# Kernel tuning notes

Measured on AMD Instinct MI355X. Metric: run time of the kernel, lower is better.

## Reference

```python
import jax, jax.numpy as jnp
import numpy as np

WINDOW = 8  # outlier_fraction = 0.125 -> 1 fp column kept per 8-wide window

# XnorBinaryLinear's STEBinary: sign in fwd, identity (straight-through) in bwd
@jax.custom_vjp
def ste_sign(x):
    return jnp.sign(x)

def _ste_fwd(x):
    return jnp.sign(x), None

def _ste_bwd(_, g):
    return (g,)

ste_sign.defvjp(_ste_fwd, _ste_bwd)


def quant_weight(w):
    # XnorBinaryLinear.quant_weight: per-row mean-center, sign, rescale by
    # detached per-row mean absolute value
    mu = jnp.mean(w, axis=-1, keepdims=True)
    wc = w - mu
    scale = jax.lax.stop_gradient(jnp.mean(jnp.abs(wc), axis=-1, keepdims=True))
    return ste_sign(wc) * scale


def binarize_except_outliers(w):
    # Binarize weight, then restore the max-|w| element of each flat 8-wide
    # window to full precision (calibration = argmax of |w| per window,
    # identical to outlier_calibration with L1 metric on first forward).
    wq = quant_weight(w)
    wv = w.reshape(-1, WINDOW)             # [n_windows, 8]
    idx = jnp.argmax(jnp.abs(wv), axis=1)  # [n_windows] outlier column per window
    mask = jnp.arange(WINDOW)[None, :] == idx[:, None]  # one-hot bool mask
    out = jnp.where(mask, wv, wq.reshape(-1, WINDOW))
    return out.reshape(w.shape)


def setup_inputs() -> dict:
    key = jax.random.key(0)
    k1, k2, k3 = jax.random.split(key, 3)
    x = jax.random.normal(k1, (4, 2048, 4096), dtype=jnp.float32)
    weight = jax.random.normal(k2, (4096, 4096), dtype=jnp.float32) * 0.02
    bias = jax.random.normal(k3, (4096,), dtype=jnp.float32) * 0.02
    return {"x": x, "weight": weight, "bias": bias}


def reference(x, weight, bias):
    w = binarize_except_outliers(weight)     # [OC, IC]
    return jnp.einsum('bsi,oi->bso', x, w) + bias
```

## Files before the change

kernel.cpp:

```cpp
#include <hip/hip_runtime.h>
#include <stdint.h>

#define M_DIM 8192
#define N_DIM 4096
#define K_DIM 4096

#define BM 128
#define BN 128
#define BK 32

typedef float v4f __attribute__((ext_vector_type(4)));
typedef __bf16 v8bf __attribute__((ext_vector_type(8)));

typedef __attribute__((address_space(3))) uint32_t lds_u32_t;
typedef const __attribute__((address_space(1))) uint32_t glb_u32_t;

__device__ inline uint16_t f2bf(float f) {
    union { float f; uint32_t u; } v; v.f = f;
    uint32_t r = v.u + 0x7fffu + ((v.u >> 16) & 1u);
    return (uint16_t)(r >> 16);
}

__global__ __launch_bounds__(256) void cvt_x(const float* __restrict__ x,
                                             uint16_t* __restrict__ xb,
                                             long long n8) {
    long long i = (long long)blockIdx.x * 256 + threadIdx.x;
    if (i >= n8) return;
    const float4* x4 = (const float4*)x;
    float4 a = x4[2 * i];
    float4 b = x4[2 * i + 1];
    union { uint16_t h[8]; uint4 u; } o;
    o.h[0] = f2bf(a.x); o.h[1] = f2bf(a.y); o.h[2] = f2bf(a.z); o.h[3] = f2bf(a.w);
    o.h[4] = f2bf(b.x); o.h[5] = f2bf(b.y); o.h[6] = f2bf(b.z); o.h[7] = f2bf(b.w);
    ((uint4*)xb)[i] = o.u;
}

__global__ __launch_bounds__(256) void make_weff(const float* __restrict__ w,
                                                 uint16_t* __restrict__ weff) {
    __shared__ double red[4];
    int row  = blockIdx.x;
    int tid  = threadIdx.x;
    int lane = tid & 63;
    int wid  = tid >> 6;

    const float* wr = w + (size_t)row * K_DIM;
    const float4* w4 = (const float4*)wr + tid * 4;
    float4 r0 = w4[0], r1 = w4[1], r2 = w4[2], r3 = w4[3];
    float v[16] = { r0.x, r0.y, r0.z, r0.w, r1.x, r1.y, r1.z, r1.w,
                    r2.x, r2.y, r2.z, r2.w, r3.x, r3.y, r3.z, r3.w };

    double s = 0.0;
#pragma unroll
    for (int j = 0; j < 16; j++) s += (double)v[j];
#pragma unroll
    for (int off = 32; off > 0; off >>= 1) s += __shfl_down(s, off);
    if (lane == 0) red[wid] = s;
    __syncthreads();
    double mu = (red[0] + red[1] + red[2] + red[3]) * (1.0 / 4096.0);
    __syncthreads();

    double sa = 0.0;
#pragma unroll
    for (int j = 0; j < 16; j++) sa += fabs((double)v[j] - mu);
#pragma unroll
    for (int off = 32; off > 0; off >>= 1) sa += __shfl_down(sa, off);
    if (lane == 0) red[wid] = sa;
    __syncthreads();
    double scale = (red[0] + red[1] + red[2] + red[3]) * (1.0 / 4096.0);

    float scf = (float)scale;
    union { uint16_t h[16]; uint4 u[2]; } o;
#pragma unroll
    for (int w2 = 0; w2 < 2; w2++) {
        int base = w2 * 8;
        int amax = 0;
        float mx = fabsf(v[base]);
#pragma unroll
        for (int j = 1; j < 8; j++) {
            float aj = fabsf(v[base + j]);
            if (aj > mx) { mx = aj; amax = j; }
        }
#pragma unroll
        for (int j = 0; j < 8; j++) {
            double wc = (double)v[base + j] - mu;
            float q = (wc > 0.0) ? scf : ((wc < 0.0) ? -scf : 0.0f);
            o.h[base + j] = f2bf((j == amax) ? v[base + j] : q);
        }
    }
    uint4* dst = (uint4*)(weff + (size_t)row * K_DIM + (size_t)tid * 16);
    dst[0] = o.u[0];
    dst[1] = o.u[1];
}

__device__ inline void async_cp16(const uint16_t* g, uint16_t* lds_uniform) {
    __builtin_amdgcn_global_load_lds((glb_u32_t*)g, (lds_u32_t*)lds_uniform, 16, 0, 0);
}

__global__ __launch_bounds__(256, 2) void gemm_bt(const uint16_t* __restrict__ A,
                                                  const uint16_t* __restrict__ B,
                                                  const float* __restrict__ bias,
                                                  float* __restrict__ C) {
    __shared__ __attribute__((aligned(16))) uint16_t As[BM * BK];
    __shared__ __attribute__((aligned(16))) uint16_t Bs[BN * BK];

    int tid  = threadIdx.x;
    int lane = tid & 63;
    int wid  = tid >> 6;
    int wm   = wid >> 1;
    int wn   = wid & 1;

    long long bm = (long long)blockIdx.y * BM;
    long long bn = (long long)blockIdx.x * BN;

    v4f acc[4][4];
#pragma unroll
    for (int i = 0; i < 4; i++)
#pragma unroll
        for (int j = 0; j < 4; j++) acc[i][j] = (v4f)(0.0f);

    const uint16_t* Ab = A + (size_t)bm * K_DIM;
    const uint16_t* Bb = B + (size_t)bn * K_DIM;

    int c0 = wid * 64 + lane;
    int c1 = c0 + 256;
    int ar0 = c0 >> 2, ac0 = (c0 & 3) * 8;
    int ar1 = c1 >> 2, ac1 = (c1 & 3) * 8;
    uint16_t* a_dst0 = As + wid * 512;
    uint16_t* a_dst1 = As + 2048 + wid * 512;
    uint16_t* b_dst0 = Bs + wid * 512;
    uint16_t* b_dst1 = Bs + 2048 + wid * 512;

    int frow = lane & 15;
    int quad = lane >> 4;

    for (int k0 = 0; k0 < K_DIM; k0 += BK) {
        async_cp16(Ab + (size_t)ar0 * K_DIM + k0 + ac0, a_dst0);
        async_cp16(Ab + (size_t)ar1 * K_DIM + k0 + ac1, a_dst1);
        async_cp16(Bb + (size_t)ar0 * K_DIM + k0 + ac0, b_dst0);
        async_cp16(Bb + (size_t)ar1 * K_DIM + k0 + ac1, b_dst1);
        __syncthreads();

        v8bf af[4], bfr[4];
#pragma unroll
        for (int i = 0; i < 4; i++)
            af[i] = *(const v8bf*)&As[(wm * 64 + i * 16 + frow) * BK + quad * 8];
#pragma unroll
        for (int j = 0; j < 4; j++)
            bfr[j] = *(const v8bf*)&Bs[(wn * 64 + j * 16 + frow) * BK + quad * 8];

#pragma unroll
        for (int i = 0; i < 4; i++)
#pragma unroll
            for (int j = 0; j < 4; j++)
                acc[i][j] = __builtin_amdgcn_mfma_f32_16x16x32_bf16(af[i], bfr[j], acc[i][j], 0, 0, 0);
        __syncthreads();
    }

    int n0 = (int)bn + wn * 64 + frow;
    int m0 = (int)bm + wm * 64 + quad * 4;
#pragma unroll
    for (int j = 0; j < 4; j++) {
        float bj = bias[n0 + j * 16];
#pragma unroll
        for (int i = 0; i < 4; i++) {
            size_t base = (size_t)(m0 + i * 16) * N_DIM + (size_t)(n0 + j * 16);
#pragma unroll
            for (int r = 0; r < 4; r++)
                C[base + (size_t)r * N_DIM] = acc[i][j][r] + bj;
        }
    }
}

extern "C" void kernel_launch(void* const* d_in, const int* in_sizes, int n_in,
                              void* d_out, int out_size, void* d_ws, size_t ws_size,
                              hipStream_t stream) {
    const float* x    = (const float*)d_in[0];
    const float* w    = (const float*)d_in[1];
    const float* bias = (const float*)d_in[2];
    float* out = (float*)d_out;

    uint16_t* xb   = (uint16_t*)d_ws;
    uint16_t* weff = (uint16_t*)((char*)d_ws + (size_t)M_DIM * K_DIM * 2);

    long long n8 = (long long)M_DIM * K_DIM / 8;
    cvt_x<<<dim3((unsigned)((n8 + 255) / 256)), dim3(256), 0, stream>>>(x, xb, n8);
    make_weff<<<dim3(N_DIM), dim3(256), 0, stream>>>(w, weff);
    gemm_bt<<<dim3(N_DIM / BN, M_DIM / BM), dim3(256), 0, stream>>>(xb, weff, bias, out);
}
```

Measured before the change: 561.4 us.

## Switch GEMM to 32x32x16 MFMA with BK=64 and XOR-swizzled LDS

Replaces the 16x16x32 bf16 MFMA tiling with 32x32x16 MFMAs, giving each wave a 2x2 grid of 32x32 accumulators. The K tile doubles to 64 to halve the number of loop iterations and barriers. LDS tiles are XOR-swizzled on 16-byte column groups to avoid bank conflicts on fragment reads. Launch bounds are raised to request 4 blocks per CU, which tightens the register budget and LDS use per block grows.

```diff
diff --git a/kernel.cpp b/kernel.cpp
--- a/kernel.cpp
+++ b/kernel.cpp
@@ -7,9 +7,9 @@
 
 #define BM 128
 #define BN 128
-#define BK 32
+#define BK 64
 
-typedef float v4f __attribute__((ext_vector_type(4)));
+typedef float v16f __attribute__((ext_vector_type(16)));
 typedef __bf16 v8bf __attribute__((ext_vector_type(8)));
 
 typedef __attribute__((address_space(3))) uint32_t lds_u32_t;
@@ -96,7 +96,7 @@
     __builtin_amdgcn_global_load_lds((glb_u32_t*)g, (lds_u32_t*)lds_uniform, 16, 0, 0);
 }
 
-__global__ __launch_bounds__(256, 2) void gemm_bt(const uint16_t* __restrict__ A,
+__global__ __launch_bounds__(256, 4) void gemm_bt(const uint16_t* __restrict__ A,
                                                   const uint16_t* __restrict__ B,
                                                   const float* __restrict__ bias,
                                                   float* __restrict__ C) {
@@ -108,65 +108,73 @@
     int wid  = tid >> 6;
     int wm   = wid >> 1;
     int wn   = wid & 1;
+    int half = lane >> 5;
+    int ml   = lane & 31;
 
     long long bm = (long long)blockIdx.y * BM;
     long long bn = (long long)blockIdx.x * BN;
 
-    v4f acc[4][4];
+    v16f acc[2][2];
 #pragma unroll
-    for (int i = 0; i < 4; i++)
+    for (int t = 0; t < 2; t++)
 #pragma unroll
-        for (int j = 0; j < 4; j++) acc[i][j] = (v4f)(0.0f);
+        for (int u = 0; u < 2; u++) acc[t][u] = (v16f)(0.0f);
 
     const uint16_t* Ab = A + (size_t)bm * K_DIM;
     const uint16_t* Bb = B + (size_t)bn * K_DIM;
 
-    int c0 = wid * 64 + lane;
-    int c1 = c0 + 256;
-    int ar0 = c0 >> 2, ac0 = (c0 & 3) * 8;
-    int ar1 = c1 >> 2, ac1 = (c1 & 3) * 8;
-    uint16_t* a_dst0 = As + wid * 512;
-    uint16_t* a_dst1 = As + 2048 + wid * 512;
-    uint16_t* b_dst0 = Bs + wid * 512;
-    uint16_t* b_dst1 = Bs + 2048 + wid * 512;
-
-    int frow = lane & 15;
-    int quad = lane >> 4;
+    int lrow = lane >> 3;
+    int cg   = (lane & 7) ^ lrow;
 
     for (int k0 = 0; k0 < K_DIM; k0 += BK) {
-        async_cp16(Ab + (size_t)ar0 * K_DIM + k0 + ac0, a_dst0);
-        async_cp16(Ab + (size_t)ar1 * K_DIM + k0 + ac1, a_dst1);
-        async_cp16(Bb + (size_t)ar0 * K_DIM + k0 + ac0, b_dst0);
-        async_cp16(Bb + (size_t)ar1 * K_DIM + k0 + ac1, b_dst1);
+#pragma unroll
+        for (int q = 0; q < 4; q++) {
+            int ib = wid * 4 + q;
+            int r  = ib * 8 + lrow;
+            const size_t go = (size_t)r * K_DIM + k0 + cg * 8;
+            async_cp16(Ab + go, As + ib * 512);
+            async_cp16(Bb + go, Bs + ib * 512);
+        }
         __syncthreads();
 
-        v8bf af[4], bfr[4];
 #pragma unroll
-        for (int i = 0; i < 4; i++)
-            af[i] = *(const v8bf*)&As[(wm * 64 + i * 16 + frow) * BK + quad * 8];
+        for (int s = 0; s < 4; s++) {
+            int cc = s * 2 + half;
+            v8bf af[2], bfv[2];
 #pragma unroll
-        for (int j = 0; j < 4; j++)
-            bfr[j] = *(const v8bf*)&Bs[(wn * 64 + j * 16 + frow) * BK + quad * 8];
-
+            for (int t = 0; t < 2; t++) {
+                int r = wm * 64 + t * 32 + ml;
+                af[t] = *(const v8bf*)&As[r * BK + ((cc ^ (r & 7)) * 8)];
+            }
 #pragma unroll
-        for (int i = 0; i < 4; i++)
+            for (int u = 0; u < 2; u++) {
+                int r = wn * 64 + u * 32 + ml;
+                bfv[u] = *(const v8bf*)&Bs[r * BK + ((cc ^ (r & 7)) * 8)];
+            }
 #pragma unroll
-            for (int j = 0; j < 4; j++)
-                acc[i][j] = __builtin_amdgcn_mfma_f32_16x16x32_bf16(af[i], bfr[j], acc[i][j], 0, 0, 0);
+            for (int t = 0; t < 2; t++)
+#pragma unroll
+                for (int u = 0; u < 2; u++)
+                    acc[t][u] = __builtin_amdgcn_mfma_f32_32x32x16_bf16(af[t], bfv[u], acc[t][u], 0, 0, 0);
+        }
         __syncthreads();
     }
 
-    int n0 = (int)bn + wn * 64 + frow;
-    int m0 = (int)bm + wm * 64 + quad * 4;
+    #pragma unroll
+    for (int u = 0; u < 2; u++) {
+        int n = (int)bn + wn * 64 + u * 32 + ml;
+        float bj = bias[n];
 #pragma unroll
-    for (int j = 0; j < 4; j++) {
-        float bj = bias[n0 + j * 16];
+        for (int t = 0; t < 2; t++) {
+            int mb = (int)bm + wm * 64 + t * 32 + half * 4;
 #pragma unroll
-        for (int i = 0; i < 4; i++) {
-            size_t base = (size_t)(m0 + i * 16) * N_DIM + (size_t)(n0 + j * 16);
+            for (int g = 0; g < 4; g++) {
 #pragma unroll
-            for (int r = 0; r < 4; r++)
-                C[base + (size_t)r * N_DIM] = acc[i][j][r] + bj;
+                for (int d = 0; d < 4; d++) {
+                    int row = mb + g * 8 + d;
+                    C[(size_t)row * N_DIM + n] = acc[t][u][g * 4 + d] + bj;
+                }
+            }
         }
     }
 }
```

Measured after the change: 529.4 us. 1.06x faster.
